# Kernel tuning notes

Hardware: AMD Instinct MI355X
Metric: run time of the kernel (lower is better)

The kernel has to match this reference:

```python
import jax, jax.numpy as jnp
import numpy as np

B, H, W, C = 4, 64, 64, 512
D = C // 8  # 64


def setup_inputs() -> dict:
    key = jax.random.key(0)
    ks = jax.random.split(key, 5)
    s_in = 1.0 / np.sqrt(C)
    s_out = 1.0 / np.sqrt(D)
    return {
        "x": jax.random.normal(ks[0], (B, H, W, C), dtype=jnp.float32),
        "Wq": jax.random.normal(ks[1], (C, D), dtype=jnp.float32) * s_in,
        "bq": jnp.zeros((D,), dtype=jnp.float32),
        "Wk": jax.random.normal(ks[2], (C, D), dtype=jnp.float32) * s_in,
        "bk": jnp.zeros((D,), dtype=jnp.float32),
        "Wv": jax.random.normal(ks[3], (C, D), dtype=jnp.float32) * s_in,
        "bv": jnp.zeros((D,), dtype=jnp.float32),
        "Wo": jax.random.normal(ks[4], (D, C), dtype=jnp.float32) * s_out,
        "bo": jnp.zeros((C,), dtype=jnp.float32),
    }


def reference(x, Wq, bq, Wk, bk, Wv, bv, Wo, bo):
    b, h, w, c = x.shape
    d = c // 8
    n = h * w
    # 1x1 convs == per-pixel matmuls; relu applied as in the original
    q = jax.nn.relu(jnp.einsum('bhwc,cd->bhwd', x, Wq) + bq).reshape(b, n, d)
    k = jax.nn.relu(jnp.einsum('bhwc,cd->bhwd', x, Wk) + bk).reshape(b, n, d)
    v = jax.nn.relu(jnp.einsum('bhwc,cd->bhwd', x, Wv) + bv).reshape(b, n, d)
    # unscaled attention: softmax(Q K^T) over the key axis (last axis)
    scores = jnp.einsum('bnd,bmd->bnm', q, k)  # [B, N, N]
    attn = jax.nn.softmax(scores, axis=-1)
    out = jnp.einsum('bnm,bmd->bnd', attn, v)  # [B, N, D]
    out = out.reshape(b, h, w, d)
    # output 1x1 conv back to C channels, then relu
    out = jax.nn.relu(jnp.einsum('bhwd,dc->bhwc', out, Wo) + bo)
    return out
```

## Files before the change

kernel.cpp:

```cpp
#include <hip/hip_runtime.h>
#include <math.h>

typedef float    f32x4  __attribute__((ext_vector_type(4)));
typedef __bf16   bf16x8 __attribute__((ext_vector_type(8)));
typedef _Float16 half8  __attribute__((ext_vector_type(8)));
typedef unsigned short ushort_t;
typedef unsigned short ushort8 __attribute__((ext_vector_type(8)));

#define NTOK  4096
#define CD    512
#define DD    64
#define BQ    256
#define BK    64
#define KSTR  72
#define PSTR  68
#define NROWS 16384
#define LOG2E 1.4426950408889634f

#define MFMAH(a, b, c) __builtin_amdgcn_mfma_f32_16x16x32_f16((a), (b), (c), 0, 0, 0)
#define MFMAB(a, b, c) __builtin_amdgcn_mfma_f32_16x16x32_bf16((a), (b), (c), 0, 0, 0)
#define EXP2(x) __builtin_amdgcn_exp2f(x)

static __device__ __forceinline__ ushort_t f2h(float f) {
    union { _Float16 h; ushort_t u; } a; a.h = (_Float16)f; return a.u;
}
static __device__ __forceinline__ ushort_t f2bf(float f) {
    union { __bf16 h; ushort_t u; } a; a.h = (__bf16)f; return a.u;
}

__global__ __launch_bounds__(256) void wprep_kernel(
    const float* __restrict__ Wq, const float* __restrict__ Wk,
    const float* __restrict__ Wv, const float* __restrict__ Wo,
    ushort_t* __restrict__ wqk, ushort_t* __restrict__ wv_t,
    ushort_t* __restrict__ woT)
{
    const int idx = blockIdx.x * 256 + threadIdx.x;
    if (idx < 192*512) {
        const int col = idx >> 9;
        const int k   = idx & 511;
        const float* W = (col < 64) ? Wq : (col < 128 ? Wk : Wv);
        const int c = col & 63;
        float wv = W[(size_t)k*DD + c];
        if (col < 64) wv *= LOG2E;
        if (col < 128) wqk[(size_t)col*CD + k] = f2h(wv);
        else           wv_t[(size_t)(col - 128)*CD + k] = f2h(wv);
    } else {
        const int i = idx - 192*512;
        const int c = i >> 6, d = i & 63;
        woT[i] = f2h(Wo[(size_t)d*CD + c]);
    }
}

__global__ __launch_bounds__(256) void qkv_gemm(
    const float* __restrict__ x,
    const ushort_t* __restrict__ wqk, const ushort_t* __restrict__ wv_t,
    const float* __restrict__ bq, const float* __restrict__ bk,
    const float* __restrict__ bv,
    ushort_t* __restrict__ qf, ushort_t* __restrict__ kf,
    ushort_t* __restrict__ vT)
{
    __shared__ __align__(16) ushort_t xs_s [32*72];
    __shared__ __align__(16) ushort_t wqk_s[128*72];
    __shared__ __align__(16) ushort_t wv_s [64*72];
    __shared__ __align__(16) ushort_t vtile[64*40];

    const int tid  = threadIdx.x;
    const int w    = tid >> 6;
    const int lane = tid & 63;
    const int l15  = lane & 15;
    const int l4   = lane >> 4;
    const int r0   = blockIdx.x * 32;

    const int rf = w & 1;
    const int cg = w >> 1;

    f32x4 acc[6];
    #pragma unroll
    for (int j = 0; j < 6; ++j) acc[j] = (f32x4){0.f,0.f,0.f,0.f};

    const int xrow = tid >> 3, xk = (tid & 7) * 8;
    const int wcol = tid >> 1, wk = (tid & 1) * 32;
    const int vcol = tid >> 2, vk = (tid & 3) * 16;

    f32x4   px0, px1;
    ushort8 pw[4], pwv[2];

    {
        const float* xp = &x[(size_t)(r0 + xrow)*CD + xk];
        px0 = *(const f32x4*)xp;  px1 = *(const f32x4*)(xp + 4);
        const ushort_t* hp = &wqk[(size_t)wcol*CD + wk];
        #pragma unroll
        for (int i = 0; i < 4; ++i) pw[i] = *(const ushort8*)(hp + 8*i);
        const ushort_t* vp = &wv_t[(size_t)vcol*CD + vk];
        pwv[0] = *(const ushort8*)vp;  pwv[1] = *(const ushort8*)(vp + 8);
    }

    for (int kt = 0; kt < 8; ++kt) {
        __syncthreads();
        {
            ushort8 h8;
            #pragma unroll
            for (int i = 0; i < 8; ++i)
                h8[i] = f2h((i < 4) ? px0[i] : px1[i-4]);
            *(ushort8*)&xs_s[xrow*72 + xk] = h8;
        }
        #pragma unroll
        for (int i = 0; i < 4; ++i)
            *(ushort8*)&wqk_s[wcol*72 + wk + 8*i] = pw[i];
        *(ushort8*)&wv_s[vcol*72 + vk]     = pwv[0];
        *(ushort8*)&wv_s[vcol*72 + vk + 8] = pwv[1];

        if (kt + 1 < 8) {
            const int ko = (kt + 1) * 64;
            const float* xp = &x[(size_t)(r0 + xrow)*CD + ko + xk];
            px0 = *(const f32x4*)xp;  px1 = *(const f32x4*)(xp + 4);
            const ushort_t* hp = &wqk[(size_t)wcol*CD + ko + wk];
            #pragma unroll
            for (int i = 0; i < 4; ++i) pw[i] = *(const ushort8*)(hp + 8*i);
            const ushort_t* vp = &wv_t[(size_t)vcol*CD + ko + vk];
            pwv[0] = *(const ushort8*)vp;  pwv[1] = *(const ushort8*)(vp + 8);
        }
        __syncthreads();

        #pragma unroll
        for (int k32 = 0; k32 < 2; ++k32) {
            const int ao = (rf*16 + l15)*72 + 8*l4 + 32*k32;
            half8 ax = *(const half8*)&xs_s[ao];
            #pragma unroll
            for (int j = 0; j < 6; ++j) {
                const int cf = 6*cg + j;
                if (cf < 8) {
                    const int bo = (16*cf + l15)*72 + 8*l4 + 32*k32;
                    half8 bw = *(const half8*)&wqk_s[bo];
                    acc[j] = MFMAH(ax, bw, acc[j]);
                } else {
                    const int bo = ((cf-8)*16 + l15)*72 + 8*l4 + 32*k32;
                    half8 bw = *(const half8*)&wv_s[bo];
                    acc[j] = MFMAH(ax, bw, acc[j]);
                }
            }
        }
    }

    #pragma unroll
    for (int j = 0; j < 6; ++j) {
        const int cf = 6*cg + j;
        const int col16 = cf*16 + l15;
        if (cf < 4) {
            const float bias = bq[col16] * LOG2E;
            #pragma unroll
            for (int r = 0; r < 4; ++r) {
                const size_t row = (size_t)(r0 + rf*16 + 4*l4 + r);
                qf[row*DD + col16] = f2h(fmaxf(acc[j][r] + bias, 0.f));
            }
        } else if (cf < 8) {
            const int kc = col16 - 64;
            const float bias = bk[kc];
            #pragma unroll
            for (int r = 0; r < 4; ++r) {
                const size_t row = (size_t)(r0 + rf*16 + 4*l4 + r);
                kf[row*DD + kc] = f2h(fmaxf(acc[j][r] + bias, 0.f));
            }
        } else {
            const int d = col16 - 128;
            const float bias = bv[d];
            #pragma unroll
            for (int r = 0; r < 4; ++r)
                vtile[d*40 + rf*16 + 4*l4 + r] =
                    f2bf(fmaxf(acc[j][r] + bias, 0.f));
        }
    }
    __syncthreads();
    {
        const int d  = tid >> 2;
        const int j8 = (tid & 3) * 8;
        const int bb   = r0 / NTOK;
        const int tok0 = r0 % NTOK;
        ushort8 vv = *(const ushort8*)&vtile[d*40 + j8];
        *(ushort8*)&vT[((size_t)bb*DD + d)*NTOK + tok0 + j8] = vv;
    }
}

__global__ __launch_bounds__(512, 4) void attn_kernel(
    const ushort_t* __restrict__ qf, const ushort_t* __restrict__ kf,
    const ushort_t* __restrict__ vT,
    float* __restrict__ o_part, float* __restrict__ l_part, int nseg)
{
    __shared__ __align__(16) ushort_t kf_s[BK*KSTR];
    __shared__ __align__(16) ushort_t vt_s[DD*KSTR];
    __shared__ __align__(16) ushort_t p_s [BQ*PSTR];

    const int tid  = threadIdx.x;
    const int w    = tid >> 6;
    const int lane = tid & 63;
    const int l15  = lane & 15;
    const int l4   = lane >> 4;

    const int p    = blockIdx.x;
    const int seg  = p % nseg;
    const int rest = p / nseg;
    const int qb   = rest & (NTOK/BQ - 1);
    const int b    = rest / (NTOK/BQ);
    const int kv0  = seg * (NTOK / nseg);
    const int tiles = (NTOK / nseg) / BK;

    half8 qfr[2][2];
    #pragma unroll
    for (int u = 0; u < 2; ++u) {
        const size_t qrow = ((size_t)b*NTOK + (size_t)qb*BQ + 32*w + 16*u + l15)*DD;
        #pragma unroll
        for (int s = 0; s < 2; ++s)
            qfr[u][s] = *(const half8*)&qf[qrow + 8*l4 + 32*s];
    }

    f32x4 acc[2][4];
    float l_run[2][4];
    #pragma unroll
    for (int u = 0; u < 2; ++u)
        #pragma unroll
        for (int nt = 0; nt < 4; ++nt) {
            acc[u][nt] = (f32x4){0.f,0.f,0.f,0.f};
            l_run[u][nt] = 0.f;
        }

    const int skey = tid >> 3;
    const int sc   = (tid & 7) * 8;
    ushort8 rgk, rgv;
    {
        rgk = *(const ushort8*)&kf[((size_t)b*NTOK + kv0 + skey)*DD + sc];
        rgv = *(const ushort8*)&vT[((size_t)b*DD + skey)*NTOK + kv0 + sc];
    }

    for (int t = 0; t < tiles; ++t) {
        __syncthreads();
        *(ushort8*)&kf_s[skey*KSTR + sc] = rgk;
        *(ushort8*)&vt_s[skey*KSTR + sc] = rgv;
        if (t + 1 < tiles) {
            rgk = *(const ushort8*)&kf[((size_t)b*NTOK + kv0 + (t+1)*BK + skey)*DD + sc];
            rgv = *(const ushort8*)&vT[((size_t)b*DD + skey)*NTOK + kv0 + (t+1)*BK + sc];
        }
        __syncthreads();

        f32x4 sv[2][4];
        #pragma unroll
        for (int u = 0; u < 2; ++u)
            #pragma unroll
            for (int nt = 0; nt < 4; ++nt) sv[u][nt] = (f32x4){0.f,0.f,0.f,0.f};
        #pragma unroll
        for (int s = 0; s < 2; ++s)
            #pragma unroll
            for (int nt = 0; nt < 4; ++nt) {
                half8 kfr = *(const half8*)&kf_s[(16*nt + l15)*KSTR + 8*l4 + 32*s];
                #pragma unroll
                for (int u = 0; u < 2; ++u)
                    sv[u][nt] = MFMAH(qfr[u][s], kfr, sv[u][nt]);
            }

        #pragma unroll
        for (int u = 0; u < 2; ++u)
            #pragma unroll
            for (int r = 0; r < 4; ++r) {
                float s0 = EXP2(sv[u][0][r]);
                float s1 = EXP2(sv[u][1][r]);
                float s2 = EXP2(sv[u][2][r]);
                float s3 = EXP2(sv[u][3][r]);
                sv[u][0][r] = s0; sv[u][1][r] = s1;
                sv[u][2][r] = s2; sv[u][3][r] = s3;
                l_run[u][r] += (s0 + s1) + (s2 + s3);
            }

        #pragma unroll
        for (int u = 0; u < 2; ++u)
            #pragma unroll
            for (int nt = 0; nt < 4; ++nt)
                #pragma unroll
                for (int r = 0; r < 4; ++r)
                    p_s[(32*w + 16*u + 4*l4 + r)*PSTR + 16*nt + l15] =
                        f2bf(sv[u][nt][r]);

        bf16x8 paf[2][2];
        #pragma unroll
        for (int u = 0; u < 2; ++u)
            #pragma unroll
            for (int s = 0; s < 2; ++s)
                paf[u][s] = *(const bf16x8*)&p_s[(32*w + 16*u + l15)*PSTR + 8*l4 + 32*s];
        #pragma unroll
        for (int s = 0; s < 2; ++s)
            #pragma unroll
            for (int nt = 0; nt < 4; ++nt) {
                bf16x8 vf = *(const bf16x8*)&vt_s[(16*nt + l15)*KSTR + 8*l4 + 32*s];
                #pragma unroll
                for (int u = 0; u < 2; ++u)
                    acc[u][nt] = MFMAB(paf[u][s], vf, acc[u][nt]);
            }
    }

    const size_t prow0 = (size_t)(seg*4 + b)*NTOK + (size_t)qb*BQ + 32*w;
    #pragma unroll
    for (int u = 0; u < 2; ++u)
        #pragma unroll
        for (int r = 0; r < 4; ++r) {
            float ls = l_run[u][r];
            ls += __shfl_xor(ls, 1);
            ls += __shfl_xor(ls, 2);
            ls += __shfl_xor(ls, 4);
            ls += __shfl_xor(ls, 8);
            const size_t row = prow0 + 16*u + 4*l4 + r;
            #pragma unroll
            for (int nt = 0; nt < 4; ++nt)
                o_part[row*DD + 16*nt + l15] = acc[u][nt][r];
            if (l15 == 0) l_part[row] = ls;
        }
}

__global__ __launch_bounds__(256) void oproj_gemm(
    const float* __restrict__ o_part, const float* __restrict__ l_part,
    const ushort_t* __restrict__ woT, const float* __restrict__ bo,
    float* __restrict__ out, int nseg)
{
    const int tid  = threadIdx.x;
    const int w    = tid >> 6;
    const int lane = tid & 63;
    const int l15  = lane & 15;
    const int l4   = lane >> 4;
    const int r0   = blockIdx.x * 32;
    const int rf   = w & 1;
    const int cg   = w >> 1;

    const int row = r0 + rf*16 + l15;
    float lsum = 0.f;
    for (int s = 0; s < nseg; ++s)
        lsum += l_part[(size_t)s*NROWS + row];
    const float inv = 1.0f / lsum;

    f32x4 acc[16];
    #pragma unroll
    for (int j = 0; j < 16; ++j) acc[j] = (f32x4){0.f,0.f,0.f,0.f};

    #pragma unroll
    for (int ks = 0; ks < 2; ++ks) {
        const int k0 = 8*l4 + 32*ks;
        float ov[8] = {0.f,0.f,0.f,0.f,0.f,0.f,0.f,0.f};
        for (int s = 0; s < nseg; ++s) {
            const float* op = &o_part[((size_t)s*NROWS + row)*DD + k0];
            const f32x4 a0 = *(const f32x4*)op;
            const f32x4 a1 = *(const f32x4*)(op + 4);
            #pragma unroll
            for (int i = 0; i < 4; ++i) {
                ov[i]   += a0[i];
                ov[i+4] += a1[i];
            }
        }
        half8 ah;
        #pragma unroll
        for (int i = 0; i < 8; ++i)
            ah[i] = (_Float16)(ov[i] * inv);
        #pragma unroll
        for (int j = 0; j < 16; ++j) {
            const int cf = cg*16 + j;
            const half8 bfr = *(const half8*)&woT[(size_t)(16*cf + l15)*DD + k0];
            acc[j] = MFMAH(ah, bfr, acc[j]);
        }
    }

    #pragma unroll
    for (int j = 0; j < 16; ++j) {
        const int col  = (cg*16 + j)*16 + l15;
        const float bias = bo[col];
        #pragma unroll
        for (int r = 0; r < 4; ++r)
            out[(size_t)(r0 + rf*16 + 4*l4 + r)*CD + col] =
                fmaxf(acc[j][r] + bias, 0.f);
    }
}

extern "C" void kernel_launch(void* const* d_in, const int* in_sizes, int n_in,
                              void* d_out, int out_size, void* d_ws, size_t ws_size,
                              hipStream_t stream) {
    const float* x  = (const float*)d_in[0];
    const float* Wq = (const float*)d_in[1];
    const float* bq = (const float*)d_in[2];
    const float* Wk = (const float*)d_in[3];
    const float* bk = (const float*)d_in[4];
    const float* Wv = (const float*)d_in[5];
    const float* bv = (const float*)d_in[6];
    const float* Wo = (const float*)d_in[7];
    const float* bo = (const float*)d_in[8];
    float* out = (float*)d_out;

    ushort_t* u = (ushort_t*)d_ws;
    const size_t SEG = (size_t)NROWS * DD;
    ushort_t* qf  = u;
    ushort_t* kf  = u + SEG;
    ushort_t* vT  = u + 2*SEG;

    ushort_t* wqk  = u + 3*SEG;
    ushort_t* wv_t = wqk + 128*512;
    ushort_t* woT  = wv_t + 64*512;
    float*    o_part = (float*)(woT + 512*64);

    const size_t base_b  = (3*SEG + 192*512 + 512*64) * sizeof(ushort_t);
    const size_t per_seg = (size_t)NROWS*DD*4 + (size_t)NROWS*4;
    int nseg = 1;
    if      (ws_size >= base_b + 8*per_seg) nseg = 8;
    else if (ws_size >= base_b + 4*per_seg) nseg = 4;
    else if (ws_size >= base_b + 2*per_seg) nseg = 2;
    float* l_part = o_part + (size_t)nseg*NROWS*DD;

    wprep_kernel<<<512, 256, 0, stream>>>(Wq, Wk, Wv, Wo, wqk, wv_t, woT);
    qkv_gemm<<<NROWS/32, 256, 0, stream>>>(x, wqk, wv_t,
                                           bq, bk, bv, qf, kf, vT);
    attn_kernel<<<(NTOK/BQ) * 4 * nseg, 512, 0, stream>>>(
        qf, kf, vT, o_part, l_part, nseg);
    oproj_gemm<<<NROWS/32, 256, 0, stream>>>(o_part, l_part, woT,
                                             bo, out, nseg);
}
```

Baseline: 75.92 us.

## Use 4 warps with 64 query rows each and store bf16 attention partials

The attention kernel now runs 256 threads per block, and each wave handles 64 query rows instead of 32. K and V fragments are loaded from LDS once per tile and reused across four row groups, which cuts LDS reads per MFMA and the cost of the block barriers. The per-segment partial outputs are written in bf16 instead of fp32, halving partial-output traffic between the attention and output-projection kernels. This raises register pressure per wave, reduces occupancy, and adds rounding error to the partial sums.

```diff
diff --git a/kernel.cpp b/kernel.cpp
--- a/kernel.cpp
+++ b/kernel.cpp
@@ -181,10 +181,10 @@
     }
 }
 
-__global__ __launch_bounds__(512, 4) void attn_kernel(
+__global__ __launch_bounds__(256, 2) void attn_kernel(
     const ushort_t* __restrict__ qf, const ushort_t* __restrict__ kf,
     const ushort_t* __restrict__ vT,
-    float* __restrict__ o_part, float* __restrict__ l_part, int nseg)
+    ushort_t* __restrict__ o_part, float* __restrict__ l_part, int nseg)
 {
     __shared__ __align__(16) ushort_t kf_s[BK*KSTR];
     __shared__ __align__(16) ushort_t vt_s[DD*KSTR];
@@ -204,100 +204,107 @@
     const int kv0  = seg * (NTOK / nseg);
     const int tiles = (NTOK / nseg) / BK;
 
-    half8 qfr[2][2];
-    #pragma unroll
-    for (int u = 0; u < 2; ++u) {
-        const size_t qrow = ((size_t)b*NTOK + (size_t)qb*BQ + 32*w + 16*u + l15)*DD;
+    half8 qfr[4][2];
+    #pragma unroll
+    for (int u = 0; u < 4; ++u) {
+        const size_t qrow = ((size_t)b*NTOK + (size_t)qb*BQ + 64*w + 16*u + l15)*DD;
         #pragma unroll
         for (int s = 0; s < 2; ++s)
             qfr[u][s] = *(const half8*)&qf[qrow + 8*l4 + 32*s];
     }
 
-    f32x4 acc[2][4];
-    float l_run[2][4];
-    #pragma unroll
-    for (int u = 0; u < 2; ++u)
+    f32x4 acc[4][4];
+    float l_run[4][4];
+    #pragma unroll
+    for (int u = 0; u < 4; ++u)
         #pragma unroll
         for (int nt = 0; nt < 4; ++nt) {
             acc[u][nt] = (f32x4){0.f,0.f,0.f,0.f};
             l_run[u][nt] = 0.f;
         }
 
-    const int skey = tid >> 3;
-    const int sc   = (tid & 7) * 8;
-    ushort8 rgk, rgv;
-    {
-        rgk = *(const ushort8*)&kf[((size_t)b*NTOK + kv0 + skey)*DD + sc];
-        rgv = *(const ushort8*)&vT[((size_t)b*DD + skey)*NTOK + kv0 + sc];
-    }
+    const int skey = tid >> 2;
+    const int sc   = (tid & 3) * 16;
+    const size_t kst = (size_t)b*NTOK*DD + (size_t)skey*DD + sc;
+    const size_t vst = (size_t)b*DD*NTOK + (size_t)skey*NTOK + sc;
+
+    ushort8 rgk0, rgk1, rgv0, rgv1;
+    rgk0 = *(const ushort8*)&kf[kst + (size_t)kv0*DD];
+    rgk1 = *(const ushort8*)&kf[kst + (size_t)kv0*DD + 8];
+    rgv0 = *(const ushort8*)&vT[vst + kv0];
+    rgv1 = *(const ushort8*)&vT[vst + kv0 + 8];
 
     for (int t = 0; t < tiles; ++t) {
         __syncthreads();
-        *(ushort8*)&kf_s[skey*KSTR + sc] = rgk;
-        *(ushort8*)&vt_s[skey*KSTR + sc] = rgv;
+        *(ushort8*)&kf_s[skey*KSTR + sc]     = rgk0;
+        *(ushort8*)&kf_s[skey*KSTR + sc + 8] = rgk1;
+        *(ushort8*)&vt_s[skey*KSTR + sc]     = rgv0;
+        *(ushort8*)&vt_s[skey*KSTR + sc + 8] = rgv1;
         if (t + 1 < tiles) {
-            rgk = *(const ushort8*)&kf[((size_t)b*NTOK + kv0 + (t+1)*BK + skey)*DD + sc];
-            rgv = *(const ushort8*)&vT[((size_t)b*DD + skey)*NTOK + kv0 + (t+1)*BK + sc];
+            const size_t ko = (size_t)(kv0 + (t+1)*BK);
+            rgk0 = *(const ushort8*)&kf[kst + ko*DD];
+            rgk1 = *(const ushort8*)&kf[kst + ko*DD + 8];
+            rgv0 = *(const ushort8*)&vT[vst + ko];
+            rgv1 = *(const ushort8*)&vT[vst + ko + 8];
         }
         __syncthreads();
 
-        f32x4 sv[2][4];
-        #pragma unroll
-        for (int u = 0; u < 2; ++u)
-            #pragma unroll
-            for (int nt = 0; nt < 4; ++nt) sv[u][nt] = (f32x4){0.f,0.f,0.f,0.f};
+        half8 kfr[2][4];
         #pragma unroll
         for (int s = 0; s < 2; ++s)
             #pragma unroll
-            for (int nt = 0; nt < 4; ++nt) {
-                half8 kfr = *(const half8*)&kf_s[(16*nt + l15)*KSTR + 8*l4 + 32*s];
+            for (int nt = 0; nt < 4; ++nt)
+                kfr[s][nt] = *(const half8*)&kf_s[(16*nt + l15)*KSTR + 8*l4 + 32*s];
+
+        #pragma unroll
+        for (int u = 0; u < 4; ++u) {
+            f32x4 sv[4];
+            #pragma unroll
+            for (int nt = 0; nt < 4; ++nt) sv[nt] = (f32x4){0.f,0.f,0.f,0.f};
+            #pragma unroll
+            for (int s = 0; s < 2; ++s)
                 #pragma unroll
-                for (int u = 0; u < 2; ++u)
-                    sv[u][nt] = MFMAH(qfr[u][s], kfr, sv[u][nt]);
-            }
-
-        #pragma unroll
-        for (int u = 0; u < 2; ++u)
+                for (int nt = 0; nt < 4; ++nt)
+                    sv[nt] = MFMAH(qfr[u][s], kfr[s][nt], sv[nt]);
             #pragma unroll
             for (int r = 0; r < 4; ++r) {
-                float s0 = EXP2(sv[u][0][r]);
-                float s1 = EXP2(sv[u][1][r]);
-                float s2 = EXP2(sv[u][2][r]);
-                float s3 = EXP2(sv[u][3][r]);
-                sv[u][0][r] = s0; sv[u][1][r] = s1;
-                sv[u][2][r] = s2; sv[u][3][r] = s3;
+                float s0 = EXP2(sv[0][r]);
+                float s1 = EXP2(sv[1][r]);
+                float s2 = EXP2(sv[2][r]);
+                float s3 = EXP2(sv[3][r]);
+                sv[0][r] = s0; sv[1][r] = s1;
+                sv[2][r] = s2; sv[3][r] = s3;
                 l_run[u][r] += (s0 + s1) + (s2 + s3);
             }
-
-        #pragma unroll
-        for (int u = 0; u < 2; ++u)
             #pragma unroll
             for (int nt = 0; nt < 4; ++nt)
                 #pragma unroll
                 for (int r = 0; r < 4; ++r)
-                    p_s[(32*w + 16*u + 4*l4 + r)*PSTR + 16*nt + l15] =
-                        f2bf(sv[u][nt][r]);
-
-        bf16x8 paf[2][2];
-        #pragma unroll
-        for (int u = 0; u < 2; ++u)
-            #pragma unroll
-            for (int s = 0; s < 2; ++s)
-                paf[u][s] = *(const bf16x8*)&p_s[(32*w + 16*u + l15)*PSTR + 8*l4 + 32*s];
+                    p_s[(64*w + 16*u + 4*l4 + r)*PSTR + 16*nt + l15] =
+                        f2bf(sv[nt][r]);
+        }
+
+        bf16x8 vfr[2][4];
         #pragma unroll
         for (int s = 0; s < 2; ++s)
             #pragma unroll
+            for (int nt = 0; nt < 4; ++nt)
+                vfr[s][nt] = *(const bf16x8*)&vt_s[(16*nt + l15)*KSTR + 8*l4 + 32*s];
+        #pragma unroll
+        for (int u = 0; u < 4; ++u) {
+            bf16x8 paf0 = *(const bf16x8*)&p_s[(64*w + 16*u + l15)*PSTR + 8*l4];
+            bf16x8 paf1 = *(const bf16x8*)&p_s[(64*w + 16*u + l15)*PSTR + 8*l4 + 32];
+            #pragma unroll
             for (int nt = 0; nt < 4; ++nt) {
-                bf16x8 vf = *(const bf16x8*)&vt_s[(16*nt + l15)*KSTR + 8*l4 + 32*s];
-                #pragma unroll
-                for (int u = 0; u < 2; ++u)
-                    acc[u][nt] = MFMAB(paf[u][s], vf, acc[u][nt]);
+                acc[u][nt] = MFMAB(paf0, vfr[0][nt], acc[u][nt]);
+                acc[u][nt] = MFMAB(paf1, vfr[1][nt], acc[u][nt]);
             }
-    }
-
-    const size_t prow0 = (size_t)(seg*4 + b)*NTOK + (size_t)qb*BQ + 32*w;
-    #pragma unroll
-    for (int u = 0; u < 2; ++u)
+        }
+    }
+
+    const size_t prow0 = (size_t)(seg*4 + b)*NTOK + (size_t)qb*BQ + 64*w;
+    #pragma unroll
+    for (int u = 0; u < 4; ++u)
         #pragma unroll
         for (int r = 0; r < 4; ++r) {
             float ls = l_run[u][r];
@@ -308,13 +315,13 @@
             const size_t row = prow0 + 16*u + 4*l4 + r;
             #pragma unroll
             for (int nt = 0; nt < 4; ++nt)
-                o_part[row*DD + 16*nt + l15] = acc[u][nt][r];
+                o_part[row*DD + 16*nt + l15] = f2bf(acc[u][nt][r]);
             if (l15 == 0) l_part[row] = ls;
         }
 }
 
 __global__ __launch_bounds__(256) void oproj_gemm(
-    const float* __restrict__ o_part, const float* __restrict__ l_part,
+    const ushort_t* __restrict__ o_part, const float* __restrict__ l_part,
     const ushort_t* __restrict__ woT, const float* __restrict__ bo,
     float* __restrict__ out, int nseg)
 {
@@ -342,14 +349,10 @@
         const int k0 = 8*l4 + 32*ks;
         float ov[8] = {0.f,0.f,0.f,0.f,0.f,0.f,0.f,0.f};
         for (int s = 0; s < nseg; ++s) {
-            const float* op = &o_part[((size_t)s*NROWS + row)*DD + k0];
-            const f32x4 a0 = *(const f32x4*)op;
-            const f32x4 a1 = *(const f32x4*)(op + 4);
-            #pragma unroll
-            for (int i = 0; i < 4; ++i) {
-                ov[i]   += a0[i];
-                ov[i+4] += a1[i];
-            }
+            const bf16x8 a = *(const bf16x8*)
+                &o_part[((size_t)s*NROWS + row)*DD + k0];
+            #pragma unroll
+            for (int i = 0; i < 8; ++i) ov[i] += (float)a[i];
         }
         half8 ah;
         #pragma unroll
@@ -397,20 +400,20 @@
     ushort_t* wqk  = u + 3*SEG;
     ushort_t* wv_t = wqk + 128*512;
     ushort_t* woT  = wv_t + 64*512;
-    float*    o_part = (float*)(woT + 512*64);
+    ushort_t* o_part = woT + 512*64;
 
     const size_t base_b  = (3*SEG + 192*512 + 512*64) * sizeof(ushort_t);
-    const size_t per_seg = (size_t)NROWS*DD*4 + (size_t)NROWS*4;
+    const size_t per_seg = (size_t)NROWS*DD*2 + (size_t)NROWS*4;
     int nseg = 1;
     if      (ws_size >= base_b + 8*per_seg) nseg = 8;
     else if (ws_size >= base_b + 4*per_seg) nseg = 4;
     else if (ws_size >= base_b + 2*per_seg) nseg = 2;
-    float* l_part = o_part + (size_t)nseg*NROWS*DD;
+    float* l_part = (float*)(o_part + (size_t)nseg*NROWS*DD);
 
     wprep_kernel<<<512, 256, 0, stream>>>(Wq, Wk, Wv, Wo, wqk, wv_t, woT);
     qkv_gemm<<<NROWS/32, 256, 0, stream>>>(x, wqk, wv_t,
                                            bq, bk, bv, qf, kf, vT);
-    attn_kernel<<<(NTOK/BQ) * 4 * nseg, 512, 0, stream>>>(
+    attn_kernel<<<(NTOK/BQ) * 4 * nseg, 256, 0, stream>>>(
         qf, kf, vT, o_part, l_part, nseg);
     oproj_gemm<<<NROWS/32, 256, 0, stream>>>(o_part, l_part, woT,
                                              bo, out, nseg);
```

Measured after the change: 71.88 us, median of 2. 5.3% less time.
